# Kernel optimization log

Hardware: AMD Instinct MI355X
Metric: run time of the kernel (lower is better)

## Reference

```python
import jax, jax.numpy as jnp
import numpy as np

OUTPUT_LEN = 180  # decoder steps, from __init__ default


def gru_cell(x, h, Wih, Whh, bih, bhh):
    """PyTorch-convention GRU cell. x:(B,in) h:(B,H) -> (B,H)."""
    gi = x @ Wih.T + bih          # (B,3H)
    gh = h @ Whh.T + bhh          # (B,3H)
    ir, iz, inn = jnp.split(gi, 3, axis=-1)
    hr, hz, hn = jnp.split(gh, 3, axis=-1)
    r = jax.nn.sigmoid(ir + hr)
    z = jax.nn.sigmoid(iz + hz)
    n = jnp.tanh(inn + r * hn)
    return (1.0 - z) * n + z * h


def setup_inputs() -> dict:
    key = jax.random.key(0)
    B, T_in, N_IN, H = 8192, 512, 2, 64
    ks = jax.random.split(key, 20)
    s = 0.05
    d = {
        "x": jax.random.normal(ks[0], (B, T_in, N_IN), jnp.float32),
        "enc_Wih0": jax.random.normal(ks[1], (3 * H, N_IN), jnp.float32) * s,
        "enc_Whh0": jax.random.normal(ks[2], (3 * H, H), jnp.float32) * s,
        "enc_bih0": jax.random.normal(ks[3], (3 * H,), jnp.float32) * s,
        "enc_bhh0": jax.random.normal(ks[4], (3 * H,), jnp.float32) * s,
        "enc_Wih1": jax.random.normal(ks[5], (3 * H, H), jnp.float32) * s,
        "enc_Whh1": jax.random.normal(ks[6], (3 * H, H), jnp.float32) * s,
        "enc_bih1": jax.random.normal(ks[7], (3 * H,), jnp.float32) * s,
        "enc_bhh1": jax.random.normal(ks[8], (3 * H,), jnp.float32) * s,
        "dec_Wih0": jax.random.normal(ks[9], (3 * H, 1), jnp.float32) * s,
        "dec_Whh0": jax.random.normal(ks[10], (3 * H, H), jnp.float32) * s,
        "dec_bih0": jax.random.normal(ks[11], (3 * H,), jnp.float32) * s,
        "dec_bhh0": jax.random.normal(ks[12], (3 * H,), jnp.float32) * s,
        "dec_Wih1": jax.random.normal(ks[13], (3 * H, H), jnp.float32) * s,
        "dec_Whh1": jax.random.normal(ks[14], (3 * H, H), jnp.float32) * s,
        "dec_bih1": jax.random.normal(ks[15], (3 * H,), jnp.float32) * s,
        "dec_bhh1": jax.random.normal(ks[16], (3 * H,), jnp.float32) * s,
        "out_W": jax.random.normal(ks[17], (1, H), jnp.float32) * s,
        "out_b": jax.random.normal(ks[18], (1,), jnp.float32) * s,
    }
    return d


def reference(x, enc_Wih0, enc_Whh0, enc_bih0, enc_bhh0,
              enc_Wih1, enc_Whh1, enc_bih1, enc_bhh1,
              dec_Wih0, dec_Whh0, dec_bih0, dec_bhh0,
              dec_Wih1, dec_Whh1, dec_bih1, dec_bhh1,
              out_W, out_b):
    B = x.shape[0]
    H = enc_Whh0.shape[1]
    h0 = jnp.zeros((B, H), x.dtype)
    h1 = jnp.zeros((B, H), x.dtype)

    # ---- encoder: 2-layer GRU over input_len steps ----
    def enc_step(carry, xt):
        h0, h1 = carry
        h0 = gru_cell(xt, h0, enc_Wih0, enc_Whh0, enc_bih0, enc_bhh0)
        h1 = gru_cell(h0, h1, enc_Wih1, enc_Whh1, enc_bih1, enc_bhh1)
        return (h0, h1), None

    (h0, h1), _ = jax.lax.scan(enc_step, (h0, h1), jnp.swapaxes(x, 0, 1))

    prev = jnp.zeros((B, 1), x.dtype)

    def dec_step(carry, _):
        h0, h1, prev = carry
        h0 = gru_cell(prev, h0, dec_Wih0, dec_Whh0, dec_bih0, dec_bhh0)
        h1 = gru_cell(h0, h1, dec_Wih1, dec_Whh1, dec_bih1, dec_bhh1)
        cv = h1 @ out_W.T + out_b          # (B,1)
        return (h0, h1, cv), cv

    _, ys = jax.lax.scan(dec_step, (h0, h1, prev), None, length=OUTPUT_LEN)
    # ys: (T, B, 1) -> (B, T, 1)
    return jnp.swapaxes(ys, 0, 1)
```

## Files before the change

### kernel.cpp

```cpp
#include <hip/hip_runtime.h>


typedef __attribute__((ext_vector_type(8))) short bf16x8;
typedef __attribute__((ext_vector_type(4))) float f32x4;

#define EXS 17
#define AHS 24
#define AHK (16*AHS + 8)

struct Params {
  const float *x;
  const float *wih0e, *bih0e, *bhh0e, *bih1e, *bhh1e;
  const float *wih0d, *bih0d, *bhh0d, *bih1d, *bhh1d;
  const float *outW, *outb;
  const unsigned short *wt;
  float *out;
};

__device__ __forceinline__ float sgm(float v) { return 1.f / (1.f + __expf(-v)); }
__device__ __forceinline__ float th(float v)  { float e = __expf(2.f * v); return 1.f - 2.f / (e + 1.f); }

__device__ __forceinline__ unsigned short rbf(float v) {
  unsigned int u = __float_as_uint(v);
  return (unsigned short)((u + 0x7fffu + ((u >> 16) & 1u)) >> 16);
}
__device__ __forceinline__ float ubf(unsigned short h) {
  return __uint_as_float((unsigned int)h << 16);
}

__device__ __forceinline__ f32x4 mfma16(bf16x8 a, bf16x8 b, f32x4 c) {
  return __builtin_amdgcn_mfma_f32_16x16x32_bf16(a, b, c, 0, 0, 0);
}

__global__ void prep_w(const float* s0, const float* s1, const float* s2,
                       const float* s3, const float* s4, const float* s5,
                       unsigned short* dst) {
  const float* srcs[6] = {s0, s1, s2, s3, s4, s5};
  const float* s = srcs[blockIdx.x];
  unsigned short* o = dst + blockIdx.x * 24576;
  for (int i = threadIdx.x; i < 24576; i += blockDim.x) {
    int e  = i & 7;
    int l  = (i >> 3) & 63;
    int sp = (i >> 9) & 1;
    int kf = (i >> 10) & 1;
    int nt = i >> 11;
    int n = nt * 16 + (l & 15);
    int k = kf * 32 + (l >> 4) * 8 + e;
    float v = s[n * 64 + k];
    unsigned short hi = rbf(v);
    unsigned short val = hi;
    if (sp) val = rbf(v - ubf(hi));
    o[i] = val;
  }
}

__global__ __launch_bounds__(256, 2) void gru_main(Params p) {
  __shared__ float exI[192 * EXS];
  __shared__ float exH[192 * EXS];
  __shared__ __align__(16) unsigned short aH0[8 * AHK];
  __shared__ __align__(16) unsigned short aH1[8 * AHK];
  __shared__ float prevs[16];

  const int tid  = threadIdx.x;
  const int lane = tid & 63;
  const int w    = tid >> 6;
  const int j    = lane;
  const int rg   = lane >> 4;
  const int rb   = lane & 15;
  const int b0   = blockIdx.x * 16;

  for (int i = tid; i < 8 * AHK; i += 256) { aH0[i] = 0; aH1[i] = 0; }
  if (tid < 16) prevs[tid] = 0.f;
  float h0own[4] = {0.f, 0.f, 0.f, 0.f}, h1own[4] = {0.f, 0.f, 0.f, 0.f};

  bf16x8 wB[3][3][2][2];

  for (int ph = 0; ph < 2; ++ph) {
#pragma unroll
    for (int m = 0; m < 3; ++m)
#pragma unroll
      for (int ntl = 0; ntl < 3; ++ntl)
#pragma unroll
        for (int kf = 0; kf < 2; ++kf)
#pragma unroll
          for (int sp = 0; sp < 2; ++sp) {
            int mtx = ph * 3 + m;
            int nt = w * 3 + ntl;
            wB[m][ntl][kf][sp] = *(const bf16x8*)(p.wt +
                ((((mtx * 12 + nt) * 2 + kf) * 2 + sp) << 9) + lane * 8);
          }
    float bi0[3], bh0[3], bi1[3], bh1[3], wxa[3], wxb[3];
#pragma unroll
    for (int g = 0; g < 3; ++g) {
      int r = g * 64 + j;
      if (ph == 0) {
        bi0[g] = p.bih0e[r]; bh0[g] = p.bhh0e[r];
        bi1[g] = p.bih1e[r]; bh1[g] = p.bhh1e[r];
        wxa[g] = p.wih0e[2 * r]; wxb[g] = p.wih0e[2 * r + 1];
      } else {
        bi0[g] = p.bih0d[r]; bh0[g] = p.bhh0d[r];
        bi1[g] = p.bih1d[r]; bh1[g] = p.bhh1d[r];
        wxa[g] = p.wih0d[r]; wxb[g] = 0.f;
      }
    }
    const float oW = p.outW[j], ob = p.outb[0];
    const int T = ph ? 180 : 512;
    __syncthreads();

    for (int t = 0; t < T; ++t) {
      float2 xx[4];
      if (ph == 0) {
#pragma unroll
        for (int i = 0; i < 4; ++i)
          xx[i] = *(const float2*)(p.x + ((size_t)(b0 + w * 4 + i) * 512 + t) * 2);
      }
      {
        bf16x8 a[2][2];
#pragma unroll
        for (int kf = 0; kf < 2; ++kf)
#pragma unroll
          for (int sp = 0; sp < 2; ++sp)
            a[kf][sp] = *(const bf16x8*)&aH0[(kf * 4 + rg) * AHK + rb * AHS + sp * 8];
#pragma unroll
        for (int ntl = 0; ntl < 3; ++ntl) {
          f32x4 acc = {0.f, 0.f, 0.f, 0.f};
#pragma unroll
          for (int kf = 0; kf < 2; ++kf) {
            acc = mfma16(a[kf][0], wB[0][ntl][kf][0], acc);
            acc = mfma16(a[kf][0], wB[0][ntl][kf][1], acc);
            acc = mfma16(a[kf][1], wB[0][ntl][kf][0], acc);
            acc = mfma16(a[kf][1], wB[0][ntl][kf][1], acc);
          }
          int row = (w * 3 + ntl) * 16 + rb;
#pragma unroll
          for (int r = 0; r < 4; ++r)
            exI[row * EXS + rg * 4 + r] = acc[r];
        }
      }
      __syncthreads();
#pragma unroll
      for (int i = 0; i < 4; ++i) {
        int b = w * 4 + i;
        float sr = exI[j * EXS + b];
        float sz = exI[(64 + j) * EXS + b];
        float sn = exI[(128 + j) * EXS + b];
        float ir, iz, inn;
        if (ph == 0) {
          ir  = bi0[0] + wxa[0] * xx[i].x + wxb[0] * xx[i].y;
          iz  = bi0[1] + wxa[1] * xx[i].x + wxb[1] * xx[i].y;
          inn = bi0[2] + wxa[2] * xx[i].x + wxb[2] * xx[i].y;
        } else {
          float pv = prevs[b];
          ir  = bi0[0] + wxa[0] * pv;
          iz  = bi0[1] + wxa[1] * pv;
          inn = bi0[2] + wxa[2] * pv;
        }
        float r = sgm(ir + bh0[0] + sr);
        float z = sgm(iz + bh0[1] + sz);
        float n = th(inn + r * (bh0[2] + sn));
        h0own[i] = (1.f - z) * n + z * h0own[i];
        unsigned short hi = rbf(h0own[i]);
        unsigned short lo = rbf(h0own[i] - ubf(hi));
        int base = (j >> 3) * AHK + b * AHS + (j & 7);
        aH0[base]     = hi;
        aH0[base + 8] = lo;
      }
      __syncthreads();
      {
        bf16x8 a[2][2];
#pragma unroll
        for (int kf = 0; kf < 2; ++kf)
#pragma unroll
          for (int sp = 0; sp < 2; ++sp)
            a[kf][sp] = *(const bf16x8*)&aH0[(kf * 4 + rg) * AHK + rb * AHS + sp * 8];
#pragma unroll
        for (int ntl = 0; ntl < 3; ++ntl) {
          f32x4 acc = {0.f, 0.f, 0.f, 0.f};
#pragma unroll
          for (int kf = 0; kf < 2; ++kf) {
            acc = mfma16(a[kf][0], wB[1][ntl][kf][0], acc);
            acc = mfma16(a[kf][0], wB[1][ntl][kf][1], acc);
            acc = mfma16(a[kf][1], wB[1][ntl][kf][0], acc);
            acc = mfma16(a[kf][1], wB[1][ntl][kf][1], acc);
          }
          int row = (w * 3 + ntl) * 16 + rb;
#pragma unroll
          for (int r = 0; r < 4; ++r)
            exI[row * EXS + rg * 4 + r] = acc[r];
        }
#pragma unroll
        for (int kf = 0; kf < 2; ++kf)
#pragma unroll
          for (int sp = 0; sp < 2; ++sp)
            a[kf][sp] = *(const bf16x8*)&aH1[(kf * 4 + rg) * AHK + rb * AHS + sp * 8];
#pragma unroll
        for (int ntl = 0; ntl < 3; ++ntl) {
          f32x4 acc = {0.f, 0.f, 0.f, 0.f};
#pragma unroll
          for (int kf = 0; kf < 2; ++kf) {
            acc = mfma16(a[kf][0], wB[2][ntl][kf][0], acc);
            acc = mfma16(a[kf][0], wB[2][ntl][kf][1], acc);
            acc = mfma16(a[kf][1], wB[2][ntl][kf][0], acc);
            acc = mfma16(a[kf][1], wB[2][ntl][kf][1], acc);
          }
          int row = (w * 3 + ntl) * 16 + rb;
#pragma unroll
          for (int r = 0; r < 4; ++r)
            exH[row * EXS + rg * 4 + r] = acc[r];
        }
      }
      __syncthreads();
      float v[4];
#pragma unroll
      for (int i = 0; i < 4; ++i) {
        int b = w * 4 + i;
        float air = exI[j * EXS + b],        ahr = exH[j * EXS + b];
        float aiz = exI[(64 + j) * EXS + b], ahz = exH[(64 + j) * EXS + b];
        float ain = exI[(128 + j) * EXS + b], ahn = exH[(128 + j) * EXS + b];
        float r = sgm(air + ahr + bi1[0] + bh1[0]);
        float z = sgm(aiz + ahz + bi1[1] + bh1[1]);
        float n = th(ain + bi1[2] + r * (bh1[2] + ahn));
        h1own[i] = (1.f - z) * n + z * h1own[i];
        unsigned short hi = rbf(h1own[i]);
        unsigned short lo = rbf(h1own[i] - ubf(hi));
        int base = (j >> 3) * AHK + b * AHS + (j & 7);
        aH1[base]     = hi;
        aH1[base + 8] = lo;
        v[i] = oW * h1own[i];
      }
      if (ph == 1) {
#pragma unroll
        for (int off = 32; off >= 1; off >>= 1)
#pragma unroll
          for (int i = 0; i < 4; ++i) v[i] += __shfl_xor(v[i], off, 64);
        if (j == 0) {
#pragma unroll
          for (int i = 0; i < 4; ++i) {
            float o = v[i] + ob;
            p.out[(size_t)(b0 + w * 4 + i) * 180 + t] = o;
            prevs[w * 4 + i] = o;
          }
        }
      }
      __syncthreads();
    }
  }
}

extern "C" void kernel_launch(void* const* d_in, const int* in_sizes, int n_in,
                              void* d_out, int out_size, void* d_ws, size_t ws_size,
                              hipStream_t stream) {
  unsigned short* wt = (unsigned short*)d_ws;

  prep_w<<<dim3(6), dim3(256), 0, stream>>>(
      (const float*)d_in[2], (const float*)d_in[5], (const float*)d_in[6],
      (const float*)d_in[10], (const float*)d_in[13], (const float*)d_in[14], wt);

  Params p;
  p.x = (const float*)d_in[0];
  p.wih0e = (const float*)d_in[1];
  p.bih0e = (const float*)d_in[3];
  p.bhh0e = (const float*)d_in[4];
  p.bih1e = (const float*)d_in[7];
  p.bhh1e = (const float*)d_in[8];
  p.wih0d = (const float*)d_in[9];
  p.bih0d = (const float*)d_in[11];
  p.bhh0d = (const float*)d_in[12];
  p.bih1d = (const float*)d_in[15];
  p.bhh1d = (const float*)d_in[16];
  p.outW = (const float*)d_in[17];
  p.outb = (const float*)d_in[18];
  p.wt = wt;
  p.out = (float*)d_out;

  gru_main<<<dim3(512), dim3(256), 0, stream>>>(p);
}
```

Before: 2.465 ms.

## Keep MFMA gate outputs in registers, double-buffer hidden state, drop exchange buffers

Each wave now owns 16 hidden units across all three gates, so the gate pre-activations come straight out of the MFMA accumulators and the exI/exH shared-memory exchange is removed. The bf16 hi/lo hidden-state buffers are double-buffered with an XOR swizzle, which cuts the barriers per step from four to two. The split-precision product now skips the lo*lo term, and the decoder output is reduced per wave and summed at the start of the next step. In exchange the activation math is spread differently across lanes, and dropping the lo*lo product slightly changes numerics.

```diff
diff --git a/kernel.cpp b/kernel.cpp
--- a/kernel.cpp
+++ b/kernel.cpp
@@ -3,10 +3,6 @@
 
 typedef __attribute__((ext_vector_type(8))) short bf16x8;
 typedef __attribute__((ext_vector_type(4))) float f32x4;
-
-#define EXS 17
-#define AHS 24
-#define AHK (16*AHS + 8)
 
 struct Params {
   const float *x;
@@ -54,23 +50,28 @@
   }
 }
 
-__global__ __launch_bounds__(256, 2) void gru_main(Params p) {
-  __shared__ float exI[192 * EXS];
-  __shared__ float exH[192 * EXS];
-  __shared__ __align__(16) unsigned short aH0[8 * AHK];
-  __shared__ __align__(16) unsigned short aH1[8 * AHK];
-  __shared__ float prevs[16];
-
-  const int tid  = threadIdx.x;
-  const int lane = tid & 63;
-  const int w    = tid >> 6;
-  const int j    = lane;
-  const int rg   = lane >> 4;
-  const int rb   = lane & 15;
-  const int b0   = blockIdx.x * 16;
-
-  for (int i = tid; i < 8 * AHK; i += 256) { aH0[i] = 0; aH1[i] = 0; }
-  if (tid < 16) prevs[tid] = 0.f;
+
+__global__ __launch_bounds__(256) __attribute__((amdgpu_waves_per_eu(2, 2)))
+void gru_main(Params p) {
+  __shared__ unsigned short aH0[2][2048];
+  __shared__ unsigned short aH1[2][2048];
+  __shared__ float pw[4][16];
+
+  const int tid = threadIdx.x;
+  const int l   = tid & 63;
+  const int w   = tid >> 6;
+  const int jc  = l & 15;
+  const int rg  = l >> 4;
+  const int j   = w * 16 + jc;
+  const int b0  = blockIdx.x * 16;
+
+  const int kfj = j >> 5, rgj = (j >> 3) & 3, ej = j & 7;
+  const int wbase = kfj * 1024 + rgj * 128 + ej;
+  const int rdb = rg * 128 + ((jc ^ rg) << 3);
+
+  for (int i = tid; i < 2048; i += 256) {
+    aH0[0][i] = 0; aH0[1][i] = 0; aH1[0][i] = 0; aH1[1][i] = 0;
+  }
   float h0own[4] = {0.f, 0.f, 0.f, 0.f}, h1own[4] = {0.f, 0.f, 0.f, 0.f};
 
   bf16x8 wB[3][3][2][2];
@@ -79,15 +80,14 @@
 #pragma unroll
     for (int m = 0; m < 3; ++m)
 #pragma unroll
-      for (int ntl = 0; ntl < 3; ++ntl)
+      for (int g = 0; g < 3; ++g)
 #pragma unroll
         for (int kf = 0; kf < 2; ++kf)
 #pragma unroll
           for (int sp = 0; sp < 2; ++sp) {
-            int mtx = ph * 3 + m;
-            int nt = w * 3 + ntl;
-            wB[m][ntl][kf][sp] = *(const bf16x8*)(p.wt +
-                ((((mtx * 12 + nt) * 2 + kf) * 2 + sp) << 9) + lane * 8);
+            int nt = g * 4 + w;
+            wB[m][g][kf][sp] = *(const bf16x8*)(p.wt +
+                (((((ph * 3 + m) * 12 + nt) * 2 + kf) * 2 + sp) << 9) + l * 8);
           }
     float bi0[3], bh0[3], bi1[3], bh1[3], wxa[3], wxb[3];
 #pragma unroll
@@ -108,141 +108,130 @@
     __syncthreads();
 
     for (int t = 0; t < T; ++t) {
-      float2 xx[4];
+      const int cur = t & 1;
+      float2 xx[4]; float prevv[4];
       if (ph == 0) {
 #pragma unroll
         for (int i = 0; i < 4; ++i)
-          xx[i] = *(const float2*)(p.x + ((size_t)(b0 + w * 4 + i) * 512 + t) * 2);
-      }
-      {
-        bf16x8 a[2][2];
-#pragma unroll
-        for (int kf = 0; kf < 2; ++kf)
-#pragma unroll
-          for (int sp = 0; sp < 2; ++sp)
-            a[kf][sp] = *(const bf16x8*)&aH0[(kf * 4 + rg) * AHK + rb * AHS + sp * 8];
-#pragma unroll
-        for (int ntl = 0; ntl < 3; ++ntl) {
-          f32x4 acc = {0.f, 0.f, 0.f, 0.f};
-#pragma unroll
-          for (int kf = 0; kf < 2; ++kf) {
-            acc = mfma16(a[kf][0], wB[0][ntl][kf][0], acc);
-            acc = mfma16(a[kf][0], wB[0][ntl][kf][1], acc);
-            acc = mfma16(a[kf][1], wB[0][ntl][kf][0], acc);
-            acc = mfma16(a[kf][1], wB[0][ntl][kf][1], acc);
+          xx[i] = *(const float2*)(p.x + ((size_t)(b0 + rg * 4 + i) * 512 + t) * 2);
+      } else {
+        if (t > 0) {
+#pragma unroll
+          for (int i = 0; i < 4; ++i)
+            prevv[i] = ob + pw[0][rg * 4 + i] + pw[1][rg * 4 + i]
+                          + pw[2][rg * 4 + i] + pw[3][rg * 4 + i];
+          if (w == 0 && jc == 0) {
+#pragma unroll
+            for (int i = 0; i < 4; ++i)
+              p.out[(size_t)(b0 + rg * 4 + i) * 180 + (t - 1)] = prevv[i];
           }
-          int row = (w * 3 + ntl) * 16 + rb;
-#pragma unroll
-          for (int r = 0; r < 4; ++r)
-            exI[row * EXS + rg * 4 + r] = acc[r];
-        }
-      }
-      __syncthreads();
+        } else {
+#pragma unroll
+          for (int i = 0; i < 4; ++i) prevv[i] = 0.f;
+        }
+      }
+      const unsigned short* h0o = aH0[cur ^ 1];
+      f32x4 aR = {0,0,0,0}, aZ = {0,0,0,0}, aN = {0,0,0,0};
+#pragma unroll
+      for (int kf = 0; kf < 2; ++kf) {
+        bf16x8 ah = *(const bf16x8*)&h0o[kf * 1024 + rdb];
+        bf16x8 al = *(const bf16x8*)&h0o[kf * 1024 + 512 + rdb];
+        aR = mfma16(ah, wB[0][0][kf][0], aR);
+        aZ = mfma16(ah, wB[0][1][kf][0], aZ);
+        aN = mfma16(ah, wB[0][2][kf][0], aN);
+        aR = mfma16(al, wB[0][0][kf][0], aR);
+        aZ = mfma16(al, wB[0][1][kf][0], aZ);
+        aN = mfma16(al, wB[0][2][kf][0], aN);
+        aR = mfma16(ah, wB[0][0][kf][1], aR);
+        aZ = mfma16(ah, wB[0][1][kf][1], aZ);
+        aN = mfma16(ah, wB[0][2][kf][1], aN);
+      }
+      unsigned short* h0n = aH0[cur];
 #pragma unroll
       for (int i = 0; i < 4; ++i) {
-        int b = w * 4 + i;
-        float sr = exI[j * EXS + b];
-        float sz = exI[(64 + j) * EXS + b];
-        float sn = exI[(128 + j) * EXS + b];
-        float ir, iz, inn;
+        float xr, xz, xn;
         if (ph == 0) {
-          ir  = bi0[0] + wxa[0] * xx[i].x + wxb[0] * xx[i].y;
-          iz  = bi0[1] + wxa[1] * xx[i].x + wxb[1] * xx[i].y;
-          inn = bi0[2] + wxa[2] * xx[i].x + wxb[2] * xx[i].y;
+          xr = bi0[0] + wxa[0] * xx[i].x + wxb[0] * xx[i].y;
+          xz = bi0[1] + wxa[1] * xx[i].x + wxb[1] * xx[i].y;
+          xn = bi0[2] + wxa[2] * xx[i].x + wxb[2] * xx[i].y;
         } else {
-          float pv = prevs[b];
-          ir  = bi0[0] + wxa[0] * pv;
-          iz  = bi0[1] + wxa[1] * pv;
-          inn = bi0[2] + wxa[2] * pv;
-        }
-        float r = sgm(ir + bh0[0] + sr);
-        float z = sgm(iz + bh0[1] + sz);
-        float n = th(inn + r * (bh0[2] + sn));
+          xr = bi0[0] + wxa[0] * prevv[i];
+          xz = bi0[1] + wxa[1] * prevv[i];
+          xn = bi0[2] + wxa[2] * prevv[i];
+        }
+        float r = sgm(xr + bh0[0] + aR[i]);
+        float z = sgm(xz + bh0[1] + aZ[i]);
+        float n = th(xn + r * (bh0[2] + aN[i]));
         h0own[i] = (1.f - z) * n + z * h0own[i];
         unsigned short hi = rbf(h0own[i]);
         unsigned short lo = rbf(h0own[i] - ubf(hi));
-        int base = (j >> 3) * AHK + b * AHS + (j & 7);
-        aH0[base]     = hi;
-        aH0[base + 8] = lo;
+        int idx = wbase + (((rg * 4 + i) ^ rgj) << 3);
+        h0n[idx] = hi; h0n[idx + 512] = lo;
       }
       __syncthreads();
-      {
-        bf16x8 a[2][2];
-#pragma unroll
-        for (int kf = 0; kf < 2; ++kf)
-#pragma unroll
-          for (int sp = 0; sp < 2; ++sp)
-            a[kf][sp] = *(const bf16x8*)&aH0[(kf * 4 + rg) * AHK + rb * AHS + sp * 8];
-#pragma unroll
-        for (int ntl = 0; ntl < 3; ++ntl) {
-          f32x4 acc = {0.f, 0.f, 0.f, 0.f};
-#pragma unroll
-          for (int kf = 0; kf < 2; ++kf) {
-            acc = mfma16(a[kf][0], wB[1][ntl][kf][0], acc);
-            acc = mfma16(a[kf][0], wB[1][ntl][kf][1], acc);
-            acc = mfma16(a[kf][1], wB[1][ntl][kf][0], acc);
-            acc = mfma16(a[kf][1], wB[1][ntl][kf][1], acc);
-          }
-          int row = (w * 3 + ntl) * 16 + rb;
-#pragma unroll
-          for (int r = 0; r < 4; ++r)
-            exI[row * EXS + rg * 4 + r] = acc[r];
-        }
-#pragma unroll
-        for (int kf = 0; kf < 2; ++kf)
-#pragma unroll
-          for (int sp = 0; sp < 2; ++sp)
-            a[kf][sp] = *(const bf16x8*)&aH1[(kf * 4 + rg) * AHK + rb * AHS + sp * 8];
-#pragma unroll
-        for (int ntl = 0; ntl < 3; ++ntl) {
-          f32x4 acc = {0.f, 0.f, 0.f, 0.f};
-#pragma unroll
-          for (int kf = 0; kf < 2; ++kf) {
-            acc = mfma16(a[kf][0], wB[2][ntl][kf][0], acc);
-            acc = mfma16(a[kf][0], wB[2][ntl][kf][1], acc);
-            acc = mfma16(a[kf][1], wB[2][ntl][kf][0], acc);
-            acc = mfma16(a[kf][1], wB[2][ntl][kf][1], acc);
-          }
-          int row = (w * 3 + ntl) * 16 + rb;
-#pragma unroll
-          for (int r = 0; r < 4; ++r)
-            exH[row * EXS + rg * 4 + r] = acc[r];
-        }
-      }
-      __syncthreads();
+      const unsigned short* h1o = aH1[cur ^ 1];
+      f32x4 iR = {0,0,0,0}, iZ = {0,0,0,0}, iN = {0,0,0,0};
+      f32x4 hR = {0,0,0,0}, hZ = {0,0,0,0}, hN = {0,0,0,0};
+#pragma unroll
+      for (int kf = 0; kf < 2; ++kf) {
+        bf16x8 gh = *(const bf16x8*)&h0n[kf * 1024 + rdb];
+        bf16x8 gl = *(const bf16x8*)&h0n[kf * 1024 + 512 + rdb];
+        bf16x8 qh = *(const bf16x8*)&h1o[kf * 1024 + rdb];
+        bf16x8 ql = *(const bf16x8*)&h1o[kf * 1024 + 512 + rdb];
+        iR = mfma16(gh, wB[1][0][kf][0], iR);
+        hR = mfma16(qh, wB[2][0][kf][0], hR);
+        iZ = mfma16(gh, wB[1][1][kf][0], iZ);
+        hZ = mfma16(qh, wB[2][1][kf][0], hZ);
+        iN = mfma16(gh, wB[1][2][kf][0], iN);
+        hN = mfma16(qh, wB[2][2][kf][0], hN);
+        iR = mfma16(gl, wB[1][0][kf][0], iR);
+        hR = mfma16(ql, wB[2][0][kf][0], hR);
+        iZ = mfma16(gl, wB[1][1][kf][0], iZ);
+        hZ = mfma16(ql, wB[2][1][kf][0], hZ);
+        iN = mfma16(gl, wB[1][2][kf][0], iN);
+        hN = mfma16(ql, wB[2][2][kf][0], hN);
+        iR = mfma16(gh, wB[1][0][kf][1], iR);
+        hR = mfma16(qh, wB[2][0][kf][1], hR);
+        iZ = mfma16(gh, wB[1][1][kf][1], iZ);
+        hZ = mfma16(qh, wB[2][1][kf][1], hZ);
+        iN = mfma16(gh, wB[1][2][kf][1], iN);
+        hN = mfma16(qh, wB[2][2][kf][1], hN);
+      }
+      unsigned short* h1n = aH1[cur];
       float v[4];
 #pragma unroll
       for (int i = 0; i < 4; ++i) {
-        int b = w * 4 + i;
-        float air = exI[j * EXS + b],        ahr = exH[j * EXS + b];
-        float aiz = exI[(64 + j) * EXS + b], ahz = exH[(64 + j) * EXS + b];
-        float ain = exI[(128 + j) * EXS + b], ahn = exH[(128 + j) * EXS + b];
-        float r = sgm(air + ahr + bi1[0] + bh1[0]);
-        float z = sgm(aiz + ahz + bi1[1] + bh1[1]);
-        float n = th(ain + bi1[2] + r * (bh1[2] + ahn));
+        float r = sgm(iR[i] + hR[i] + bi1[0] + bh1[0]);
+        float z = sgm(iZ[i] + hZ[i] + bi1[1] + bh1[1]);
+        float n = th(iN[i] + bi1[2] + r * (bh1[2] + hN[i]));
         h1own[i] = (1.f - z) * n + z * h1own[i];
         unsigned short hi = rbf(h1own[i]);
         unsigned short lo = rbf(h1own[i] - ubf(hi));
-        int base = (j >> 3) * AHK + b * AHS + (j & 7);
-        aH1[base]     = hi;
-        aH1[base + 8] = lo;
+        int idx = wbase + (((rg * 4 + i) ^ rgj) << 3);
+        h1n[idx] = hi; h1n[idx + 512] = lo;
         v[i] = oW * h1own[i];
       }
       if (ph == 1) {
 #pragma unroll
-        for (int off = 32; off >= 1; off >>= 1)
+        for (int off = 1; off < 16; off <<= 1)
 #pragma unroll
           for (int i = 0; i < 4; ++i) v[i] += __shfl_xor(v[i], off, 64);
-        if (j == 0) {
-#pragma unroll
-          for (int i = 0; i < 4; ++i) {
-            float o = v[i] + ob;
-            p.out[(size_t)(b0 + w * 4 + i) * 180 + t] = o;
-            prevs[w * 4 + i] = o;
-          }
+        if (jc == 0) {
+#pragma unroll
+          for (int i = 0; i < 4; ++i) pw[w][rg * 4 + i] = v[i];
         }
       }
       __syncthreads();
+    }
+    if (ph == 1) {
+      if (w == 0 && jc == 0) {
+#pragma unroll
+        for (int i = 0; i < 4; ++i) {
+          float fv = ob + pw[0][rg * 4 + i] + pw[1][rg * 4 + i]
+                        + pw[2][rg * 4 + i] + pw[3][rg * 4 + i];
+          p.out[(size_t)(b0 + rg * 4 + i) * 180 + 179] = fv;
+        }
+      }
     }
   }
 }
```

New measurement: 2.154 ms. 1.14x faster.
